# Kernel tuning notes

Hardware: AMD Instinct MI355X
Metric: run time of the kernel (lower is better)

## Reference

```python
import jax, jax.numpy as jnp
import numpy as np

B, P, L, M, L_EVAL = 8, 16, 256, 16, 2048
T_MAX = 100.0


def setup_inputs() -> dict:
    key = jax.random.key(0)
    k1, k2, k3, k4, k5 = jax.random.split(key, 5)
    # sorted event times per path (Hawkes event streams are ordered)
    event_times = jnp.sort(jax.random.uniform(k1, (B, P, L), dtype=jnp.float32) * T_MAX, axis=-1)
    # parameters are assumed already positive (post-softplus) -> uniform [0,1)
    mu = jax.random.uniform(k2, (B, M, P, L), dtype=jnp.float32)
    alpha = jax.random.uniform(k3, (B, M, P, L), dtype=jnp.float32)
    beta = jax.random.uniform(k4, (B, M, P, L), dtype=jnp.float32)
    query_times = jax.random.uniform(k5, (B, P, L_EVAL), dtype=jnp.float32) * T_MAX
    return {"query_times": query_times, "event_times": event_times,
            "mu": mu, "alpha": alpha, "beta": beta}


def reference(query_times, event_times, mu, alpha, beta):
    # query_times: [B,P,Le]; event_times: [B,P,L]; mu/alpha/beta: [B,M,P,L]
    b, m, p, l = mu.shape
    le = query_times.shape[-1]
    # index of latest event strictly before each query time (mask + max, as original)
    past_mask = event_times[:, :, None, :] < query_times[:, :, :, None]  # [B,P,Le,L]
    idx = jnp.arange(l, dtype=jnp.int32)
    last_idx = jnp.max(jnp.where(past_mask, idx, -1), axis=-1)            # [B,P,Le]
    ci = jnp.clip(last_idx, 0, None)
    gi = jnp.broadcast_to(ci[:, None, :, :], (b, m, p, le))
    mu_last = jnp.take_along_axis(mu, gi, axis=3)
    alpha_last = jnp.take_along_axis(alpha, gi, axis=3)
    beta_last = jnp.take_along_axis(beta, gi, axis=3)
    t_last = jnp.take_along_axis(event_times, ci, axis=2)                 # [B,P,Le]
    t_last = jnp.where(last_idx == -1, jnp.zeros_like(t_last), t_last)
    delta_t = (query_times - t_last)[:, None, :, :]                       # [B,1,P,Le]
    base = mu_last + (alpha_last - mu_last) * jnp.exp(-beta_last * delta_t)
    return jax.nn.softplus(base)                                          # [B,M,P,Le]
```

## Files before the change

### kernel.cpp

```cpp
#include <hip/hip_runtime.h>
#include <float.h>

#define BB  8
#define PP  16
#define LL  256
#define MM  16
#define LE  2048
#define TILE 512
#define THREADS 256

__global__ __launch_bounds__(THREADS) void hawkes_intensity_kernel(
    const float* __restrict__ qt,
    const float* __restrict__ ev,
    const float* __restrict__ mu,
    const float* __restrict__ alpha,
    const float* __restrict__ beta,
    float* __restrict__ out)
{
    __shared__ float ev_s[LL + 1];
    __shared__ float mu_s[MM * LL];
    __shared__ float al_s[MM * LL];
    __shared__ float be_s[MM * LL];

    const int tiles_per_bp = LE / TILE;
    const int bp   = blockIdx.x / tiles_per_bp;
    const int tile = blockIdx.x % tiles_per_bp;
    const int b = bp / PP;
    const int p = bp % PP;
    const int t = threadIdx.x;

    ev_s[t] = ev[bp * LL + t];
    if (t == 0) ev_s[LL] = FLT_MAX;

    {
        const float4* mu4 = (const float4*)mu;
        const float4* al4 = (const float4*)alpha;
        const float4* be4 = (const float4*)beta;
        float4* mus4 = (float4*)mu_s;
        float4* als4 = (float4*)al_s;
        float4* bes4 = (float4*)be_s;
        #pragma unroll
        for (int i = t; i < MM * LL / 4; i += THREADS) {
            const int m  = i >> 6;
            const int l4 = i & 63;
            const int g  = ((b * MM + m) * PP + p) * (LL / 4) + l4;
            mus4[i] = mu4[g];
            als4[i] = al4[g];
            bes4[i] = be4[g];
        }
    }
    __syncthreads();

    const int le0 = tile * TILE;
    const float* qrow = qt + bp * LE + le0;

    #pragma unroll
    for (int k = 0; k < TILE; k += THREADS) {
        const int le = le0 + k + t;
        const float q = qrow[k + t];

        int lo = 0, hi = LL;
        #pragma unroll
        for (int s = 0; s < 9; ++s) {
            const int mid = (lo + hi) >> 1;
            if (ev_s[mid] < q) lo = mid + 1; else hi = mid;
        }
        const int cnt = lo;
        const int ci  = (cnt > 0) ? (cnt - 1) : 0;
        const float t_last = (cnt > 0) ? ev_s[ci] : 0.0f;
        const float dt = q - t_last;

        int o = ((b * MM) * PP + p) * LE + le;
        #pragma unroll
        for (int m = 0; m < MM; ++m) {
            const float mm = mu_s[m * LL + ci];
            const float aa = al_s[m * LL + ci];
            const float bb = be_s[m * LL + ci];
            const float e  = __expf(-bb * dt);
            const float base = mm + (aa - mm) * e;
            out[o] = __logf(1.0f + __expf(base));
            o += PP * LE;
        }
    }
}

extern "C" void kernel_launch(void* const* d_in, const int* in_sizes, int n_in,
                              void* d_out, int out_size, void* d_ws, size_t ws_size,
                              hipStream_t stream) {
    const float* qt    = (const float*)d_in[0];
    const float* ev    = (const float*)d_in[1];
    const float* mu    = (const float*)d_in[2];
    const float* alpha = (const float*)d_in[3];
    const float* beta  = (const float*)d_in[4];
    float* out = (float*)d_out;

    const int nblocks = (BB * PP) * (LE / TILE);
    hawkes_intensity_kernel<<<nblocks, THREADS, 0, stream>>>(qt, ev, mu, alpha, beta, out);
}
```

Before: 78.02 us.

## Replace binary search with two-level scan and pack precomputed parameters in LDS

Swaps the 9-step dependent binary search for a two-level linear scan: 16 block-maximum compares, then one 16-element window read as four float4 loads, which also yields t_last directly. Parameters are stored in LDS as (mu, alpha-mu) pairs and -beta, so each output needs one fma plus fewer LDS loads. Blocks grow to 512 threads with one query per thread, which halves the per-thread work and doubles the number of parameter-staging passes into LDS. The staging loop now uses scalar global loads instead of float4 loads, which could make the load phase slower.

```diff
diff --git a/kernel.cpp b/kernel.cpp
--- a/kernel.cpp
+++ b/kernel.cpp
@@ -1,15 +1,23 @@
 #include <hip/hip_runtime.h>
-#include <float.h>
 
 #define BB  8
 #define PP  16
 #define LL  256
 #define MM  16
 #define LE  2048
-#define TILE 512
-#define THREADS 256
+#define THREADS 512
+#define TILE THREADS
 
-__global__ __launch_bounds__(THREADS) void hawkes_intensity_kernel(
+__device__ __forceinline__ void acc4(const float4 v, const float q, int& cin, float& tl)
+{
+    bool c;
+    c = (v.x < q); cin += c; tl = c ? fmaxf(tl, v.x) : tl;
+    c = (v.y < q); cin += c; tl = c ? fmaxf(tl, v.y) : tl;
+    c = (v.z < q); cin += c; tl = c ? fmaxf(tl, v.z) : tl;
+    c = (v.w < q); cin += c; tl = c ? fmaxf(tl, v.w) : tl;
+}
+
+__global__ __launch_bounds__(THREADS, 4) void hawkes_intensity_kernel(
     const float* __restrict__ qt,
     const float* __restrict__ ev,
     const float* __restrict__ mu,
@@ -17,10 +25,9 @@
     const float* __restrict__ beta,
     float* __restrict__ out)
 {
-    __shared__ float ev_s[LL + 1];
-    __shared__ float mu_s[MM * LL];
-    __shared__ float al_s[MM * LL];
-    __shared__ float be_s[MM * LL];
+    __shared__ float2 pma_s[MM * LL];
+    __shared__ float  pnb_s[MM * LL];
+    __shared__ __align__(16) float ev_s[LL];
 
     const int tiles_per_bp = LE / TILE;
     const int bp   = blockIdx.x / tiles_per_bp;
@@ -29,58 +36,59 @@
     const int p = bp % PP;
     const int t = threadIdx.x;
 
-    ev_s[t] = ev[bp * LL + t];
-    if (t == 0) ev_s[LL] = FLT_MAX;
+    const int le = tile * TILE + t;
+    const float q = qt[bp * LE + le];
 
-    {
-        const float4* mu4 = (const float4*)mu;
-        const float4* al4 = (const float4*)alpha;
-        const float4* be4 = (const float4*)beta;
-        float4* mus4 = (float4*)mu_s;
-        float4* als4 = (float4*)al_s;
-        float4* bes4 = (float4*)be_s;
-        #pragma unroll
-        for (int i = t; i < MM * LL / 4; i += THREADS) {
-            const int m  = i >> 6;
-            const int l4 = i & 63;
-            const int g  = ((b * MM + m) * PP + p) * (LL / 4) + l4;
-            mus4[i] = mu4[g];
-            als4[i] = al4[g];
-            bes4[i] = be4[g];
-        }
+    if (t < LL) ev_s[t] = ev[bp * LL + t];
+
+    #pragma unroll
+    for (int i = t; i < MM * LL; i += THREADS) {
+        const int m = i >> 8;
+        const int l = i & (LL - 1);
+        const int g = ((b * MM + m) * PP + p) * LL + l;
+        const float mm = mu[g];
+        const float aa = alpha[g];
+        const float bb = beta[g];
+        pma_s[i] = make_float2(mm, aa - mm);
+        pnb_s[i] = -bb;
     }
     __syncthreads();
 
-    const int le0 = tile * TILE;
-    const float* qrow = qt + bp * LE + le0;
+    int F = 0;
+    float tl = 0.0f;
+    #pragma unroll
+    for (int j = 0; j < 16; ++j) {
+        const float r = ev_s[j * 16 + 15];
+        const bool c = (r < q);
+        F += c;
+        tl = c ? fmaxf(tl, r) : tl;
+    }
+    const int Fc = (F < 16) ? F : 15;
 
+    const float4* ev4 = (const float4*)ev_s;
+    const float4 w0 = ev4[Fc * 4 + 0];
+    const float4 w1 = ev4[Fc * 4 + 1];
+    const float4 w2 = ev4[Fc * 4 + 2];
+    const float4 w3 = ev4[Fc * 4 + 3];
+    int cin = 0;
+    acc4(w0, q, cin, tl);
+    acc4(w1, q, cin, tl);
+    acc4(w2, q, cin, tl);
+    acc4(w3, q, cin, tl);
+
+    const int cnt = Fc * 16 + cin;
+    const int ci  = (cnt > 0) ? (cnt - 1) : 0;
+    const float dt = q - tl;
+
+    int o = (b * MM * PP + p) * LE + le;
     #pragma unroll
-    for (int k = 0; k < TILE; k += THREADS) {
-        const int le = le0 + k + t;
-        const float q = qrow[k + t];
-
-        int lo = 0, hi = LL;
-        #pragma unroll
-        for (int s = 0; s < 9; ++s) {
-            const int mid = (lo + hi) >> 1;
-            if (ev_s[mid] < q) lo = mid + 1; else hi = mid;
-        }
-        const int cnt = lo;
-        const int ci  = (cnt > 0) ? (cnt - 1) : 0;
-        const float t_last = (cnt > 0) ? ev_s[ci] : 0.0f;
-        const float dt = q - t_last;
-
-        int o = ((b * MM) * PP + p) * LE + le;
-        #pragma unroll
-        for (int m = 0; m < MM; ++m) {
-            const float mm = mu_s[m * LL + ci];
-            const float aa = al_s[m * LL + ci];
-            const float bb = be_s[m * LL + ci];
-            const float e  = __expf(-bb * dt);
-            const float base = mm + (aa - mm) * e;
-            out[o] = __logf(1.0f + __expf(base));
-            o += PP * LE;
-        }
+    for (int m = 0; m < MM; ++m) {
+        const float2 pm = pma_s[(m << 8) | ci];
+        const float  nb = pnb_s[(m << 8) | ci];
+        const float  e  = __expf(nb * dt);
+        const float  base = fmaf(pm.y, e, pm.x);
+        out[o] = __logf(1.0f + __expf(base));
+        o += PP * LE;
     }
 }
 
```

After: 78.32 us (median of 2 runs). About the same (+0.4%).
